# Performance work log

Hardware: AMD Instinct MI355X
Metric: run time of the kernel (lower is better)

Reference implementation:

```python
import jax, jax.numpy as jnp
import numpy as np

B = 32768          # batch
M = 128            # m_spa, embedding dim
N_TAB = 26         # number of sparse tables
N_ROWS = 100000    # rows per table
LN_BOT = [13, 512, 256, 128]
LN_TOP = [479, 1024, 1024, 1]  # 479 = 128 + 27*26/2

# strictly-lower-triangle indices of the (1+N_TAB) x (1+N_TAB) interaction matrix,
# in the same row-major order as the torch list-comprehension.
_LI, _LJ = np.tril_indices(N_TAB + 1, k=-1)


def _mlp_params(key, ln):
    ws, bs = [], []
    for i in range(len(ln) - 1):
        n, m = ln[i], ln[i + 1]
        key, k1, k2 = jax.random.split(key, 3)
        ws.append(jax.random.normal(k1, (m, n), jnp.float32) * np.sqrt(2.0 / (m + n)))
        bs.append(jax.random.normal(k2, (m,), jnp.float32) * np.sqrt(1.0 / m))
    return ws, bs


def setup_inputs() -> dict:
    key = jax.random.key(0)
    kd, ki, ke, kb, kt = jax.random.split(key, 5)
    dense_x = jax.random.normal(kd, (B, LN_BOT[0]), jnp.float32)
    lS_i = jax.random.randint(ki, (N_TAB, B), 0, N_ROWS, dtype=jnp.int64)
    lS_o = jnp.tile(jnp.arange(B, dtype=jnp.int64), (N_TAB, 1))  # one index per bag
    bound = np.sqrt(1.0 / N_ROWS)
    emb_W = jax.random.uniform(ke, (N_TAB, N_ROWS, M), jnp.float32, -bound, bound)
    bw, bb = _mlp_params(kb, LN_BOT)
    tw, tb = _mlp_params(kt, LN_TOP)
    return {
        "dense_x": dense_x, "lS_i": lS_i, "lS_o": lS_o, "emb_W": emb_W,
        "bot_w0": bw[0], "bot_b0": bb[0], "bot_w1": bw[1], "bot_b1": bb[1],
        "bot_w2": bw[2], "bot_b2": bb[2],
        "top_w0": tw[0], "top_b0": tb[0], "top_w1": tw[1], "top_b1": tb[1],
        "top_w2": tw[2], "top_b2": tb[2],
    }


def _forward(dense_x, lS_i, emb_W,
             bot_w0, bot_b0, bot_w1, bot_b1, bot_w2, bot_b2,
             top_w0, top_b0, top_w1, top_b1, top_w2, top_b2):
    # bottom MLP (all ReLU, sigmoid_bot = -1)
    x = jax.nn.relu(dense_x @ bot_w0.T + bot_b0)
    x = jax.nn.relu(x @ bot_w1.T + bot_b1)
    x = jax.nn.relu(x @ bot_w2.T + bot_b2)                      # [B, M]
    # embedding lookups; offsets are arange(B) -> sum-pool of a single index == gather
    ly = jax.vmap(lambda W, idx: W[idx])(emb_W, lS_i)           # [N_TAB, B, M]
    # pairwise feature interaction
    T = jnp.concatenate([x[:, None, :], jnp.transpose(ly, (1, 0, 2))], axis=1)  # [B, 27, M]
    Z = jnp.einsum('bid,bjd->bij', T, T)                        # [B, 27, 27]
    Zflat = Z[:, _LI, _LJ]                                      # [B, 351]
    R = jnp.concatenate([x, Zflat], axis=1)                     # [B, 479]
    # top MLP (ReLU, ReLU, Sigmoid at layer index 2)
    z = jax.nn.relu(R @ top_w0.T + top_b0)
    z = jax.nn.relu(z @ top_w1.T + top_b1)
    p = jax.nn.sigmoid(z @ top_w2.T + top_b2)                   # [B, 1]
    return p  # loss_threshold == 0.0 -> no clamp


def reference(dense_x, lS_i, lS_o, emb_W,
              bot_w0, bot_b0, bot_w1, bot_b1, bot_w2, bot_b2,
              top_w0, top_b0, top_w1, top_b1, top_w2, top_b2):
    del lS_o  # offsets = arange(B): one index per bag, pooling is identity
    return _forward(dense_x, lS_i, emb_W,
                    bot_w0, bot_b0, bot_w1, bot_b1, bot_w2, bot_b2,
                    top_w0, top_b0, top_w1, top_b1, top_w2, top_b2)
```

## Files before the change

### kernel.cpp

```cpp
#include <hip/hip_runtime.h>

typedef unsigned short u16;
typedef unsigned int   u32;
typedef __attribute__((ext_vector_type(4))) float f32x4;
typedef __attribute__((ext_vector_type(8))) short bf16x8;
typedef __attribute__((ext_vector_type(4))) unsigned short u16x4;

__device__ __forceinline__ u16 f2bf(float f) {
  u32 u = __float_as_uint(f);
  u = (u + 0x7FFFu + ((u >> 16) & 1u)) >> 16;
  return (u16)u;
}
__device__ __forceinline__ float bf2f(u16 h) {
  return __uint_as_float(((u32)h) << 16);
}

#define GLDS16(gptr, lptr)                                      \
  __builtin_amdgcn_global_load_lds(                             \
      (const __attribute__((address_space(1))) void*)(gptr),    \
      (__attribute__((address_space(3))) void*)(lptr), 16, 0, 0)

#define BARRIER                                                 \
  do {                                                          \
    asm volatile("" ::: "memory");                              \
    __builtin_amdgcn_s_barrier();                               \
    asm volatile("" ::: "memory");                              \
  } while (0)
#define WAITLGKM0 asm volatile("s_waitcnt lgkmcnt(0)" ::: "memory")
#define WAITVM2   asm volatile("s_waitcnt vmcnt(2)" ::: "memory")
#define WAITVM0   asm volatile("s_waitcnt vmcnt(0)" ::: "memory")
#define PRIO1 __builtin_amdgcn_s_setprio(1)
#define PRIO0 __builtin_amdgcn_s_setprio(0)

#define PREP_TOTAL (6656 + 131072 + 32768 + 524288 + 1048576 + 32768)
__global__ __launch_bounds__(256) void prep(
    const float* __restrict__ bw0, const float* __restrict__ bw1,
    const float* __restrict__ bw2, const float* __restrict__ tw0,
    const float* __restrict__ tw1,
    float* __restrict__ w0T, u16* __restrict__ W1B, u16* __restrict__ W2B,
    u16* __restrict__ TW0B, u16* __restrict__ TW1B, float* __restrict__ DOT) {
  int i = blockIdx.x * 256 + threadIdx.x;
  if (i < 6656) {
    int k = i >> 9, n = i & 511;
    w0T[i] = bw0[n * 13 + k];
    return;
  }
  i -= 6656;
  if (i < 131072) { W1B[i] = f2bf(bw1[i]); return; }
  i -= 131072;
  if (i < 32768) { W2B[i] = f2bf(bw2[i]); return; }
  i -= 32768;
  if (i < 524288) {
    int r = i >> 9, k = i & 511;
    TW0B[i] = (k < 479) ? f2bf(tw0[r * 479 + k]) : (u16)0;
    return;
  }
  i -= 524288;
  if (i < 1048576) { TW1B[i] = f2bf(tw1[i]); return; }
  i -= 1048576;
  if (i < 32768) DOT[i] = 0.f;
}

__global__ __launch_bounds__(256) void bot0(const float* __restrict__ dense,
                                            const float* __restrict__ w0T,
                                            const float* __restrict__ b0,
                                            u16* __restrict__ x1) {
  const int t = blockIdx.x * 256 + threadIdx.x;
  const int b = t >> 9, n = t & 511;
  const float* dr = dense + (size_t)b * 13;
  float s = b0[n];
#pragma unroll
  for (int k = 0; k < 13; ++k) s = fmaf(dr[k], w0T[k * 512 + n], s);
  x1[t] = f2bf(fmaxf(s, 0.f));
}

__global__ __launch_bounds__(256) void gemm_bt_relu(
    const u16* __restrict__ A, const u16* __restrict__ W,
    const float* __restrict__ bias, u16* __restrict__ C,
    int M, int N, int K) {
  __shared__ u16 Al[128 * 32];
  __shared__ u16 Bl[128 * 32];
  const int tid = threadIdx.x;
  const int wave = tid >> 6, lane = tid & 63;
  const int ntn = N >> 7;
  const int bm = blockIdx.x / ntn, bn = blockIdx.x % ntn;
  const int wm = (wave >> 1) << 6, wn = (wave & 1) << 6;
  const int fr = lane & 15, fq = lane >> 4;

  const int srow = wave * 16 + (lane >> 2);
  const int scol = (lane & 3) * 8;
  const u16* ag0 = A + (size_t)(bm * 128 + srow) * K + scol;
  const u16* ag1 = ag0 + (size_t)64 * K;
  const u16* wg0 = W + (size_t)(bn * 128 + srow) * K + scol;
  const u16* wg1 = wg0 + (size_t)64 * K;
  u16* la0 = &Al[(wave * 16) * 32];
  u16* la1 = &Al[(64 + wave * 16) * 32];
  u16* lb0 = &Bl[(wave * 16) * 32];
  u16* lb1 = &Bl[(64 + wave * 16) * 32];

  f32x4 acc[4][4] = {};

  for (int kt = 0; kt < K; kt += 32) {
    __syncthreads();
    GLDS16(ag0 + kt, la0);
    GLDS16(ag1 + kt, la1);
    GLDS16(wg0 + kt, lb0);
    GLDS16(wg1 + kt, lb1);
    __syncthreads();
    bf16x8 af[4], bfv[4];
#pragma unroll
    for (int i = 0; i < 4; ++i) {
      af[i]  = *(const bf16x8*)&Al[(wm + i * 16 + fr) * 32 + fq * 8];
      bfv[i] = *(const bf16x8*)&Bl[(wn + i * 16 + fr) * 32 + fq * 8];
    }
#pragma unroll
    for (int i = 0; i < 4; ++i)
#pragma unroll
      for (int j = 0; j < 4; ++j)
        acc[i][j] = __builtin_amdgcn_mfma_f32_16x16x32_bf16(af[i], bfv[j],
                                                            acc[i][j], 0, 0, 0);
  }

  const int crow0 = bm * 128 + wm, ccol0 = bn * 128 + wn;
#pragma unroll
  for (int i = 0; i < 4; ++i) {
#pragma unroll
    for (int j = 0; j < 4; ++j) {
      const int col = ccol0 + j * 16 + fr;
      const float bv = bias[col];
#pragma unroll
      for (int rr = 0; rr < 4; ++rr) {
        const int row = crow0 + i * 16 + fq * 4 + rr;
        float v = acc[i][j][rr] + bv;
        v = fmaxf(v, 0.f);
        C[(size_t)row * N + col] = f2bf(v);
      }
    }
  }
}

#define LDA4(dst, FB, BUFE)                                                    \
  _Pragma("unroll") for (int f = 0; f < 4; ++f)                                \
  _Pragma("unroll") for (int ks = 0; ks < 2; ++ks)                             \
    dst[f][ks] = *(const bf16x8*)&lds[(BUFE) +                                 \
        (wm * 128 + (FB) * 16 + f * 16 + fr) * 64 +                            \
        ((ks * 4 + fq) ^ fr7) * 8];

#define LDB2(dst, GB, BUFE)                                                    \
  _Pragma("unroll") for (int g = 0; g < 2; ++g)                                \
  _Pragma("unroll") for (int ks = 0; ks < 2; ++ks)                             \
    dst[g][ks] = *(const bf16x8*)&lds[(BUFE) + 16384 +                         \
        (wn * 64 + (GB) * 16 + g * 16 + fr) * 64 +                             \
        ((ks * 4 + fq) ^ fr7) * 8];

#define MFQ(FB, GB, va, vb)                                                    \
  _Pragma("unroll") for (int f = 0; f < 4; ++f)                                \
  _Pragma("unroll") for (int g = 0; g < 2; ++g)                                \
  _Pragma("unroll") for (int ks = 0; ks < 2; ++ks)                             \
    acc[(FB) + f][(GB) + g] = __builtin_amdgcn_mfma_f32_16x16x32_bf16(         \
        va[f][ks], vb[g][ks], acc[(FB) + f][(GB) + g], 0, 0, 0);

template <int FUSE>
__global__ __launch_bounds__(512, 2) void gemm256(
    const u16* __restrict__ Ap, const u16* __restrict__ Wp,
    const float* __restrict__ bias, u16* __restrict__ C,
    const float* __restrict__ w2, float* __restrict__ dotacc,
    int N, int K) {
  __shared__ u16 lds[65536];
  const int tid = threadIdx.x;
  const int wave = tid >> 6, lane = tid & 63;
  const int wm = wave >> 2, wn = wave & 3;
  const int fr = lane & 15, fq = lane >> 4, fr7 = fr & 7;
  const int nkt = K >> 6, NP = nkt >> 1;

  const int nwg = gridDim.x;
  const int swz = (blockIdx.x & 7) * (nwg >> 3) + (blockIdx.x >> 3);
  const int ntn = N >> 8;
  const int bm = swz / ntn, bn = swz % ntn;

  auto stageH = [&](int tile, int half) {
    const int isB = half >> 1;
    const int h128 = half & 1;
    const u16* mat = isB ? Wp : Ap;
    const int brow0 = (isB ? bn : bm) * 256 + h128 * 128;
    u16* lb = lds + (tile & 1) * 32768 + isB * 16384 + h128 * 8192 + wave * 512;
    const int sl = lane >> 3;
    const int ch = (lane & 7) ^ sl;
    const u16* g = mat + (size_t)(brow0 + wave * 8 + sl) * K + tile * 64 + ch * 8;
    GLDS16(g, lb);
    GLDS16(g + (size_t)64 * K, lb + 4096);
  };

  f32x4 acc[8][4] = {};

  stageH(0, 0); stageH(0, 1); stageH(0, 2); stageH(0, 3);
  stageH(1, 0);
  WAITVM2;
  BARRIER;

  for (int p = 0; p < NP; ++p) {
    const int todd = 2 * p + 1, t2 = 2 * p + 2, t3 = 2 * p + 3;
    const bool last = (p == NP - 1);
    bf16x8 va[4][2], vb0[2][2], vb1[2][2];

    LDA4(va, 0, 0); LDB2(vb0, 0, 0);
    stageH(todd, 1);
    BARRIER; WAITLGKM0; PRIO1; MFQ(0, 0, va, vb0); PRIO0; BARRIER;
    LDB2(vb1, 2, 0);
    stageH(todd, 2);
    BARRIER; WAITLGKM0; PRIO1; MFQ(0, 2, va, vb1); PRIO0; BARRIER;
    LDA4(va, 4, 0);
    stageH(todd, 3);
    BARRIER; WAITLGKM0; PRIO1; MFQ(4, 0, va, vb0); PRIO0; BARRIER;
    if (t2 < nkt) stageH(t2, 0);
    BARRIER; PRIO1; MFQ(4, 2, va, vb1); PRIO0;
    if (last) { WAITVM0; } else { WAITVM2; }
    BARRIER;

    LDA4(va, 0, 32768); LDB2(vb0, 0, 32768);
    if (t2 < nkt) stageH(t2, 1);
    BARRIER; WAITLGKM0; PRIO1; MFQ(0, 0, va, vb0); PRIO0; BARRIER;
    LDB2(vb1, 2, 32768);
    if (t2 < nkt) stageH(t2, 2);
    BARRIER; WAITLGKM0; PRIO1; MFQ(0, 2, va, vb1); PRIO0; BARRIER;
    LDA4(va, 4, 32768);
    if (t2 < nkt) stageH(t2, 3);
    BARRIER; WAITLGKM0; PRIO1; MFQ(4, 0, va, vb0); PRIO0; BARRIER;
    if (t3 < nkt) stageH(t3, 0);
    BARRIER; PRIO1; MFQ(4, 2, va, vb1); PRIO0;
    if (!last) { WAITVM2; }
    BARRIER;
  }

  const int r0 = bm * 256 + wm * 128;
  const int c0 = bn * 256 + wn * 64;
  if (FUSE) {
    float bv[4], wv[4];
#pragma unroll
    for (int g = 0; g < 4; ++g) {
      const int col = c0 + g * 16 + fr;
      bv[g] = bias[col];
      wv[g] = w2[col];
    }
#pragma unroll
    for (int f = 0; f < 8; ++f) {
#pragma unroll
      for (int rr = 0; rr < 4; ++rr) {
        float s = 0.f;
#pragma unroll
        for (int g = 0; g < 4; ++g)
          s += fmaxf(acc[f][g][rr] + bv[g], 0.f) * wv[g];
#pragma unroll
        for (int off = 8; off >= 1; off >>= 1) s += __shfl_xor(s, off, 64);
        if (fr == 0)
          atomicAdd(&dotacc[r0 + f * 16 + fq * 4 + rr], s);
      }
    }
  } else {
#pragma unroll
    for (int g = 0; g < 4; ++g) {
      const int col = c0 + g * 16 + fr;
      const float bvv = bias[col];
#pragma unroll
      for (int f = 0; f < 8; ++f)
#pragma unroll
        for (int rr = 0; rr < 4; ++rr) {
          const int row = r0 + f * 16 + fq * 4 + rr;
          C[(size_t)row * N + col] = f2bf(fmaxf(acc[f][g][rr] + bvv, 0.f));
        }
    }
  }
}

__global__ __launch_bounds__(256) void interact(const float* __restrict__ emb,
                                                const int* __restrict__ lsi,
                                                const u16* __restrict__ x3,
                                                u16* __restrict__ R) {
  __shared__ u16 lds[4 * 32 * 128];
  const int tid = threadIdx.x;
  const int b0 = blockIdx.x * 4;

  {
    u32* lz = (u32*)lds;
#pragma unroll
    for (int z = 0; z < 5; ++z) {
      int i = z * 256 + tid;
      int s = i / 320, o = i - s * 320;
      lz[s * 2048 + 1728 + o] = 0u;
    }
  }
  if (tid < 64) {
    int s = tid >> 4, l = tid & 15;
    *(bf16x8*)&lds[(s * 32) * 128 + l * 8] =
        *(const bf16x8*)&x3[(size_t)(b0 + s) * 128 + l * 8];
  }
  {
    const int lane32 = tid & 31;
    const int item0 = tid >> 5;
#pragma unroll
    for (int p = 0; p < 13; ++p) {
      int w = p * 8 + item0;
      int s = w / 26, t = w - s * 26;
      int idx = lsi[t * 32768 + b0 + s];
      const float* er = emb + ((size_t)t * 100000 + (size_t)idx) * 128 + lane32 * 4;
      f32x4 u = *(const f32x4*)er;
      u16x4 q;
      q[0] = f2bf(u[0]); q[1] = f2bf(u[1]); q[2] = f2bf(u[2]); q[3] = f2bf(u[3]);
      int r = t + 1;
      int chunk = (lane32 >> 1) ^ (r & 7);
      *(u16x4*)&lds[(s * 32 + r) * 128 + chunk * 8 + (lane32 & 1) * 4] = q;
    }
  }
  __syncthreads();

  const int wave = tid >> 6, lane = tid & 63;
  const int fr = lane & 15, fq = lane >> 4;
  const u16* ls = &lds[wave * 4096];
  u16* Rb = R + (size_t)(b0 + wave) * 512;

  *(u32*)&Rb[lane * 2] = *(const u32*)&ls[lane * 2];
  if (lane < 33) Rb[479 + lane] = 0;

  bf16x8 tf[2][4];
#pragma unroll
  for (int mi = 0; mi < 2; ++mi) {
    const int r = mi * 16 + fr;
#pragma unroll
    for (int ks = 0; ks < 4; ++ks) {
      const int chunk = (ks * 4 + fq) ^ (r & 7);
      tf[mi][ks] = *(const bf16x8*)&ls[r * 128 + chunk * 8];
    }
  }

  f32x4 acc[2][2] = {};
#pragma unroll
  for (int ks = 0; ks < 4; ++ks)
#pragma unroll
    for (int mi = 0; mi < 2; ++mi)
#pragma unroll
      for (int ni = 0; ni < 2; ++ni)
        acc[mi][ni] = __builtin_amdgcn_mfma_f32_16x16x32_bf16(
            tf[mi][ks], tf[ni][ks], acc[mi][ni], 0, 0, 0);

#pragma unroll
  for (int mi = 0; mi < 2; ++mi)
#pragma unroll
    for (int ni = 0; ni < 2; ++ni)
#pragma unroll
      for (int rr = 0; rr < 4; ++rr) {
        const int i = mi * 16 + fq * 4 + rr;
        const int j = ni * 16 + fr;
        if (i < 27 && j < i)
          Rb[128 + (i * (i - 1)) / 2 + j] = f2bf(acc[mi][ni][rr]);
      }
}

__global__ __launch_bounds__(256) void sig_k(const float* __restrict__ accv,
                                             const float* __restrict__ b2,
                                             float* __restrict__ out, int n) {
  int i = blockIdx.x * 256 + threadIdx.x;
  if (i < n) out[i] = 1.f / (1.f + expf(-(accv[i] + b2[0])));
}

extern "C" void kernel_launch(void* const* d_in, const int* in_sizes, int n_in,
                              void* d_out, int out_size, void* d_ws,
                              size_t ws_size, hipStream_t stream) {
  const float* dense = (const float*)d_in[0];
  const int*   lsi   = (const int*)d_in[1];
  const float* emb = (const float*)d_in[3];
  const float* bw0 = (const float*)d_in[4];
  const float* bb0 = (const float*)d_in[5];
  const float* bw1 = (const float*)d_in[6];
  const float* bb1 = (const float*)d_in[7];
  const float* bw2 = (const float*)d_in[8];
  const float* bb2 = (const float*)d_in[9];
  const float* tw0 = (const float*)d_in[10];
  const float* tb0 = (const float*)d_in[11];
  const float* tw1 = (const float*)d_in[12];
  const float* tb1 = (const float*)d_in[13];
  const float* tw2 = (const float*)d_in[14];
  const float* tb2 = (const float*)d_in[15];

  char* ws = (char*)d_ws;
  u16* W1B  = (u16*)ws; ws += (size_t)256 * 512 * 2;
  u16* W2B  = (u16*)ws; ws += (size_t)128 * 256 * 2;
  u16* TW0B = (u16*)ws; ws += (size_t)1024 * 512 * 2;
  u16* TW1B = (u16*)ws; ws += (size_t)1024 * 1024 * 2;
  float* DOT = (float*)ws; ws += (size_t)32768 * 4;
  float* W0T = (float*)ws; ws += (size_t)13 * 512 * 4;
  u16* X3   = (u16*)ws; ws += (size_t)32768 * 128 * 2;
  u16* SA   = (u16*)ws; ws += (size_t)32768 * 1024 * 2;
  u16* SB   = (u16*)ws; ws += (size_t)32768 * 1024 * 2;

  prep<<<(PREP_TOTAL + 255) / 256, 256, 0, stream>>>(
      bw0, bw1, bw2, tw0, tw1, W0T, W1B, W2B, TW0B, TW1B, DOT);

  bot0<<<65536, 256, 0, stream>>>(dense, W0T, bb0, SA);
  gemm_bt_relu<<<512, 256, 0, stream>>>(SA, W1B, bb1, SB, 32768, 256, 512);
  gemm_bt_relu<<<256, 256, 0, stream>>>(SB, W2B, bb2, X3, 32768, 128, 256);
  interact<<<8192, 256, 0, stream>>>(emb, lsi, X3, SA);
  gemm256<0><<<512, 512, 0, stream>>>(SA, TW0B, tb0, SB, nullptr, nullptr,
                                      1024, 512);
  gemm256<1><<<512, 512, 0, stream>>>(SB, TW1B, tb1, nullptr, tw2, DOT,
                                      1024, 1024);
  sig_k<<<128, 256, 0, stream>>>(DOT, tb2, (float*)d_out, 32768);
}
```

Before: 310.6 us.

## Pipeline interaction and top-MLP GEMMs across batch chunks in combined launches

Splits the batch into four chunks of 8192 rows. Each combined 'pipe' kernel runs the interaction for the next chunk, the first top-MLP GEMM for the current chunk and the fused second GEMM plus dot product for the previous chunk, picking the role by block index. This overlaps the memory-bound embedding gather with the compute-bound GEMMs and fills the GPU better between stages. In exchange the top GEMMs use the smaller 128-tile body instead of the 256-tile kernel in the pipelined stages, and there are more launches.

```diff
diff --git a/kernel.cpp b/kernel.cpp
--- a/kernel.cpp
+++ b/kernel.cpp
@@ -74,16 +74,16 @@
   x1[t] = f2bf(fmaxf(s, 0.f));
 }
 
-__global__ __launch_bounds__(256) void gemm_bt_relu(
-    const u16* __restrict__ A, const u16* __restrict__ W,
+template <int FUSE>
+__device__ __forceinline__ void g128_body(
+    u16* lds, const u16* __restrict__ A, const u16* __restrict__ W,
     const float* __restrict__ bias, u16* __restrict__ C,
-    int M, int N, int K) {
-  __shared__ u16 Al[128 * 32];
-  __shared__ u16 Bl[128 * 32];
+    const float* __restrict__ w2, float* __restrict__ dotacc,
+    int bm, int bn, int N, int K) {
+  u16* Al = lds;
+  u16* Bl = lds + 4096;
   const int tid = threadIdx.x;
   const int wave = tid >> 6, lane = tid & 63;
-  const int ntn = N >> 7;
-  const int bm = blockIdx.x / ntn, bn = blockIdx.x % ntn;
   const int wm = (wave >> 1) << 6, wn = (wave & 1) << 6;
   const int fr = lane & 15, fq = lane >> 4;
 
@@ -122,21 +122,172 @@
   }
 
   const int crow0 = bm * 128 + wm, ccol0 = bn * 128 + wn;
-#pragma unroll
-  for (int i = 0; i < 4; ++i) {
+  if (FUSE) {
+    float bv[4], wv[4];
 #pragma unroll
     for (int j = 0; j < 4; ++j) {
       const int col = ccol0 + j * 16 + fr;
-      const float bv = bias[col];
+      bv[j] = bias[col];
+      wv[j] = w2[col];
+    }
+#pragma unroll
+    for (int i = 0; i < 4; ++i)
 #pragma unroll
       for (int rr = 0; rr < 4; ++rr) {
-        const int row = crow0 + i * 16 + fq * 4 + rr;
-        float v = acc[i][j][rr] + bv;
-        v = fmaxf(v, 0.f);
-        C[(size_t)row * N + col] = f2bf(v);
+        float s = 0.f;
+#pragma unroll
+        for (int j = 0; j < 4; ++j)
+          s += fmaxf(acc[i][j][rr] + bv[j], 0.f) * wv[j];
+#pragma unroll
+        for (int off = 8; off >= 1; off >>= 1) s += __shfl_xor(s, off, 64);
+        if (fr == 0)
+          atomicAdd(&dotacc[crow0 + i * 16 + fq * 4 + rr], s);
       }
-    }
-  }
+  } else {
+#pragma unroll
+    for (int i = 0; i < 4; ++i)
+#pragma unroll
+      for (int j = 0; j < 4; ++j) {
+        const int col = ccol0 + j * 16 + fr;
+        const float bvv = bias[col];
+#pragma unroll
+        for (int rr = 0; rr < 4; ++rr) {
+          const int row = crow0 + i * 16 + fq * 4 + rr;
+          C[(size_t)row * N + col] = f2bf(fmaxf(acc[i][j][rr] + bvv, 0.f));
+        }
+      }
+  }
+}
+
+__global__ __launch_bounds__(256) void gemm_bt_relu(
+    const u16* __restrict__ A, const u16* __restrict__ W,
+    const float* __restrict__ bias, u16* __restrict__ C, int N, int K) {
+  __shared__ u16 lds[8192];
+  const int ntn = N >> 7;
+  g128_body<0>(lds, A, W, bias, C, nullptr, nullptr, blockIdx.x / ntn,
+               blockIdx.x % ntn, N, K);
+}
+
+__device__ __forceinline__ void interact_body(u16* lds,
+                                              const float* __restrict__ emb,
+                                              const int* __restrict__ lsi,
+                                              const u16* __restrict__ x3,
+                                              u16* __restrict__ R, int b0) {
+  const int tid = threadIdx.x;
+  {
+    u32* lz = (u32*)lds;
+#pragma unroll
+    for (int z = 0; z < 5; ++z) {
+      int i = z * 256 + tid;
+      int s = i / 320, o = i - s * 320;
+      lz[s * 2048 + 1728 + o] = 0u;
+    }
+  }
+  if (tid < 64) {
+    int s = tid >> 4, l = tid & 15;
+    *(bf16x8*)&lds[(s * 32) * 128 + l * 8] =
+        *(const bf16x8*)&x3[(size_t)(b0 + s) * 128 + l * 8];
+  }
+  {
+    const int lane32 = tid & 31;
+    const int item0 = tid >> 5;
+#pragma unroll
+    for (int p = 0; p < 13; ++p) {
+      int w = p * 8 + item0;
+      int s = w / 26, t = w - s * 26;
+      int idx = lsi[t * 32768 + b0 + s];
+      const float* er =
+          emb + ((size_t)t * 100000 + (size_t)idx) * 128 + lane32 * 4;
+      f32x4 u = *(const f32x4*)er;
+      u16x4 q;
+      q[0] = f2bf(u[0]); q[1] = f2bf(u[1]); q[2] = f2bf(u[2]); q[3] = f2bf(u[3]);
+      int r = t + 1;
+      int chunk = (lane32 >> 1) ^ (r & 7);
+      *(u16x4*)&lds[(s * 32 + r) * 128 + chunk * 8 + (lane32 & 1) * 4] = q;
+    }
+  }
+  __syncthreads();
+
+  const int wave = tid >> 6, lane = tid & 63;
+  const int fr = lane & 15, fq = lane >> 4;
+  const u16* ls = &lds[wave * 4096];
+  u16* Rb = R + (size_t)(b0 + wave) * 512;
+
+  *(u32*)&Rb[lane * 2] = *(const u32*)&ls[lane * 2];
+  if (lane < 33) Rb[479 + lane] = 0;
+
+  bf16x8 tf[2][4];
+#pragma unroll
+  for (int mi = 0; mi < 2; ++mi) {
+    const int r = mi * 16 + fr;
+#pragma unroll
+    for (int ks = 0; ks < 4; ++ks) {
+      const int chunk = (ks * 4 + fq) ^ (r & 7);
+      tf[mi][ks] = *(const bf16x8*)&ls[r * 128 + chunk * 8];
+    }
+  }
+
+  f32x4 acc[2][2] = {};
+#pragma unroll
+  for (int ks = 0; ks < 4; ++ks)
+#pragma unroll
+    for (int mi = 0; mi < 2; ++mi)
+#pragma unroll
+      for (int ni = 0; ni < 2; ++ni)
+        acc[mi][ni] = __builtin_amdgcn_mfma_f32_16x16x32_bf16(
+            tf[mi][ks], tf[ni][ks], acc[mi][ni], 0, 0, 0);
+
+#pragma unroll
+  for (int mi = 0; mi < 2; ++mi)
+#pragma unroll
+    for (int ni = 0; ni < 2; ++ni)
+#pragma unroll
+      for (int rr = 0; rr < 4; ++rr) {
+        const int i = mi * 16 + fq * 4 + rr;
+        const int j = ni * 16 + fr;
+        if (i < 27 && j < i)
+          Rb[128 + (i * (i - 1)) / 2 + j] = f2bf(acc[mi][ni][rr]);
+      }
+}
+
+__global__ __launch_bounds__(256) void interact_k(const float* __restrict__ emb,
+                                                  const int* __restrict__ lsi,
+                                                  const u16* __restrict__ x3,
+                                                  u16* __restrict__ R,
+                                                  int bOff) {
+  __shared__ u16 lds[16384];
+  interact_body(lds, emb, lsi, x3, R, bOff + blockIdx.x * 4);
+}
+
+__global__ __launch_bounds__(256) void pipe(
+    const float* __restrict__ emb, const int* __restrict__ lsi,
+    const u16* __restrict__ x3, u16* __restrict__ R, int ibase,
+    int iA, int nZ1, int nZ2,
+    const u16* __restrict__ A1, u16* __restrict__ C1,
+    const u16* __restrict__ W1, const float* __restrict__ b1,
+    const u16* __restrict__ A2, const u16* __restrict__ W2,
+    const float* __restrict__ b2, const float* __restrict__ w2v,
+    float* __restrict__ dot) {
+  __shared__ u16 lds[16384];
+  int bid = blockIdx.x;
+  if (bid < iA) {
+    interact_body(lds, emb, lsi, x3, R, ibase + bid * 4);
+    return;
+  }
+  bid -= iA;
+  if (bid < nZ1) {
+    g128_body<0>(lds, A1, W1, b1, C1, nullptr, nullptr, bid >> 3, bid & 7,
+                 1024, 512);
+    return;
+  }
+  bid -= nZ1;
+  if (bid < nZ2) {
+    g128_body<1>(lds, A2, W2, b2, nullptr, w2v, dot, bid >> 3, bid & 7,
+                 1024, 1024);
+    return;
+  }
+  bid -= nZ2;
+  interact_body(lds, emb, lsi, x3, R, ibase + (iA + bid) * 4);
 }
 
 #define LDA4(dst, FB, BUFE)                                                    \
@@ -270,89 +421,6 @@
         }
     }
   }
-}
-
-__global__ __launch_bounds__(256) void interact(const float* __restrict__ emb,
-                                                const int* __restrict__ lsi,
-                                                const u16* __restrict__ x3,
-                                                u16* __restrict__ R) {
-  __shared__ u16 lds[4 * 32 * 128];
-  const int tid = threadIdx.x;
-  const int b0 = blockIdx.x * 4;
-
-  {
-    u32* lz = (u32*)lds;
-#pragma unroll
-    for (int z = 0; z < 5; ++z) {
-      int i = z * 256 + tid;
-      int s = i / 320, o = i - s * 320;
-      lz[s * 2048 + 1728 + o] = 0u;
-    }
-  }
-  if (tid < 64) {
-    int s = tid >> 4, l = tid & 15;
-    *(bf16x8*)&lds[(s * 32) * 128 + l * 8] =
-        *(const bf16x8*)&x3[(size_t)(b0 + s) * 128 + l * 8];
-  }
-  {
-    const int lane32 = tid & 31;
-    const int item0 = tid >> 5;
-#pragma unroll
-    for (int p = 0; p < 13; ++p) {
-      int w = p * 8 + item0;
-      int s = w / 26, t = w - s * 26;
-      int idx = lsi[t * 32768 + b0 + s];
-      const float* er = emb + ((size_t)t * 100000 + (size_t)idx) * 128 + lane32 * 4;
-      f32x4 u = *(const f32x4*)er;
-      u16x4 q;
-      q[0] = f2bf(u[0]); q[1] = f2bf(u[1]); q[2] = f2bf(u[2]); q[3] = f2bf(u[3]);
-      int r = t + 1;
-      int chunk = (lane32 >> 1) ^ (r & 7);
-      *(u16x4*)&lds[(s * 32 + r) * 128 + chunk * 8 + (lane32 & 1) * 4] = q;
-    }
-  }
-  __syncthreads();
-
-  const int wave = tid >> 6, lane = tid & 63;
-  const int fr = lane & 15, fq = lane >> 4;
-  const u16* ls = &lds[wave * 4096];
-  u16* Rb = R + (size_t)(b0 + wave) * 512;
-
-  *(u32*)&Rb[lane * 2] = *(const u32*)&ls[lane * 2];
-  if (lane < 33) Rb[479 + lane] = 0;
-
-  bf16x8 tf[2][4];
-#pragma unroll
-  for (int mi = 0; mi < 2; ++mi) {
-    const int r = mi * 16 + fr;
-#pragma unroll
-    for (int ks = 0; ks < 4; ++ks) {
-      const int chunk = (ks * 4 + fq) ^ (r & 7);
-      tf[mi][ks] = *(const bf16x8*)&ls[r * 128 + chunk * 8];
-    }
-  }
-
-  f32x4 acc[2][2] = {};
-#pragma unroll
-  for (int ks = 0; ks < 4; ++ks)
-#pragma unroll
-    for (int mi = 0; mi < 2; ++mi)
-#pragma unroll
-      for (int ni = 0; ni < 2; ++ni)
-        acc[mi][ni] = __builtin_amdgcn_mfma_f32_16x16x32_bf16(
-            tf[mi][ks], tf[ni][ks], acc[mi][ni], 0, 0, 0);
-
-#pragma unroll
-  for (int mi = 0; mi < 2; ++mi)
-#pragma unroll
-    for (int ni = 0; ni < 2; ++ni)
-#pragma unroll
-      for (int rr = 0; rr < 4; ++rr) {
-        const int i = mi * 16 + fq * 4 + rr;
-        const int j = ni * 16 + fr;
-        if (i < 27 && j < i)
-          Rb[128 + (i * (i - 1)) / 2 + j] = f2bf(acc[mi][ni][rr]);
-      }
 }
 
 __global__ __launch_bounds__(256) void sig_k(const float* __restrict__ accv,
@@ -392,16 +460,32 @@
   u16* SA   = (u16*)ws; ws += (size_t)32768 * 1024 * 2;
   u16* SB   = (u16*)ws; ws += (size_t)32768 * 1024 * 2;
 
+  const int CH = 8192;
+  auto SAc = [&](int c) { return SA + (size_t)c * CH * 512; };
+  auto SBc = [&](int c) { return SB + (size_t)c * CH * 1024; };
+
   prep<<<(PREP_TOTAL + 255) / 256, 256, 0, stream>>>(
       bw0, bw1, bw2, tw0, tw1, W0T, W1B, W2B, TW0B, TW1B, DOT);
 
   bot0<<<65536, 256, 0, stream>>>(dense, W0T, bb0, SA);
-  gemm_bt_relu<<<512, 256, 0, stream>>>(SA, W1B, bb1, SB, 32768, 256, 512);
-  gemm_bt_relu<<<256, 256, 0, stream>>>(SB, W2B, bb2, X3, 32768, 128, 256);
-  interact<<<8192, 256, 0, stream>>>(emb, lsi, X3, SA);
-  gemm256<0><<<512, 512, 0, stream>>>(SA, TW0B, tb0, SB, nullptr, nullptr,
-                                      1024, 512);
-  gemm256<1><<<512, 512, 0, stream>>>(SB, TW1B, tb1, nullptr, tw2, DOT,
-                                      1024, 1024);
+  gemm_bt_relu<<<512, 256, 0, stream>>>(SA, W1B, bb1, SB, 256, 512);
+  gemm_bt_relu<<<256, 256, 0, stream>>>(SB, W2B, bb2, X3, 128, 256);
+
+  interact_k<<<2048, 256, 0, stream>>>(emb, lsi, X3, SA, 0);
+  pipe<<<512 + 512 + 0 + 1536, 256, 0, stream>>>(
+      emb, lsi, X3, SA, 1 * CH, 512, 512, 0,
+      SAc(0), SBc(0), TW0B, tb0, nullptr, TW1B, tb1, tw2, nullptr);
+  pipe<<<512 + 512 + 512 + 1536, 256, 0, stream>>>(
+      emb, lsi, X3, SA, 2 * CH, 512, 512, 512,
+      SAc(1), SBc(1), TW0B, tb0, SBc(0), TW1B, tb1, tw2, DOT + 0 * CH);
+  pipe<<<512 + 512 + 512 + 1536, 256, 0, stream>>>(
+      emb, lsi, X3, SA, 3 * CH, 512, 512, 512,
+      SAc(2), SBc(2), TW0B, tb0, SBc(1), TW1B, tb1, tw2, DOT + 1 * CH);
+  gemm256<0><<<128, 512, 0, stream>>>(SAc(3), TW0B, tb0, SBc(3), nullptr,
+                                      nullptr, 1024, 512);
+  gemm256<1><<<128, 512, 0, stream>>>(SBc(2), TW1B, tb1, nullptr, tw2,
+                                      DOT + 2 * CH, 1024, 1024);
+  gemm256<1><<<128, 512, 0, stream>>>(SBc(3), TW1B, tb1, nullptr, tw2,
+                                      DOT + 3 * CH, 1024, 1024);
   sig_k<<<128, 256, 0, stream>>>(DOT, tb2, (float*)d_out, 32768);
 }
```

After: 361.3 us. 1.16x slower.

## Fuse last bottom-MLP layer into interaction kernel using scalar FMA

Applied to the files above, without the earlier changes.

Removes the separate 256->128 bottom GEMM launch and its X3 intermediate by computing that layer inside the interaction kernel. Each thread computes two output columns for one sample with scalar bf16->fp32 FMAs, reading the activation row and two weight rows from global memory. This saves one launch and a round trip through global memory, but replaces an MFMA GEMM with scalar math and re-reads the 64KB weight matrix in every block. It also adds a long serial dot-product loop before the barrier.

```diff
diff --git a/kernel.cpp b/kernel.cpp
--- a/kernel.cpp
+++ b/kernel.cpp
@@ -272,10 +272,12 @@
   }
 }
 
-__global__ __launch_bounds__(256) void interact(const float* __restrict__ emb,
-                                                const int* __restrict__ lsi,
-                                                const u16* __restrict__ x3,
-                                                u16* __restrict__ R) {
+__global__ __launch_bounds__(256) void interact3(const float* __restrict__ emb,
+                                                 const int* __restrict__ lsi,
+                                                 const u16* __restrict__ x2,
+                                                 const u16* __restrict__ W2B,
+                                                 const float* __restrict__ b2v,
+                                                 u16* __restrict__ R) {
   __shared__ u16 lds[4 * 32 * 128];
   const int tid = threadIdx.x;
   const int b0 = blockIdx.x * 4;
@@ -289,11 +291,6 @@
       lz[s * 2048 + 1728 + o] = 0u;
     }
   }
-  if (tid < 64) {
-    int s = tid >> 4, l = tid & 15;
-    *(bf16x8*)&lds[(s * 32) * 128 + l * 8] =
-        *(const bf16x8*)&x3[(size_t)(b0 + s) * 128 + l * 8];
-  }
   {
     const int lane32 = tid & 31;
     const int item0 = tid >> 5;
@@ -302,7 +299,8 @@
       int w = p * 8 + item0;
       int s = w / 26, t = w - s * 26;
       int idx = lsi[t * 32768 + b0 + s];
-      const float* er = emb + ((size_t)t * 100000 + (size_t)idx) * 128 + lane32 * 4;
+      const float* er =
+          emb + ((size_t)t * 100000 + (size_t)idx) * 128 + lane32 * 4;
       f32x4 u = *(const f32x4*)er;
       u16x4 q;
       q[0] = f2bf(u[0]); q[1] = f2bf(u[1]); q[2] = f2bf(u[2]); q[3] = f2bf(u[3]);
@@ -311,6 +309,32 @@
       *(u16x4*)&lds[(s * 32 + r) * 128 + chunk * 8 + (lane32 & 1) * 4] = q;
     }
   }
+  {
+    const int s = tid >> 6, c0 = (tid & 63) * 2;
+    const u16* xr = x2 + (size_t)(b0 + s) * 256;
+    const u16* wr0 = W2B + (size_t)c0 * 256;
+    const u16* wr1 = wr0 + 256;
+    float a0 = b2v[c0], a1 = b2v[c0 + 1];
+#pragma unroll
+    for (int k = 0; k < 256; k += 8) {
+      bf16x8 xv  = *(const bf16x8*)&xr[k];
+      bf16x8 wv0 = *(const bf16x8*)&wr0[k];
+      bf16x8 wv1 = *(const bf16x8*)&wr1[k];
+#pragma unroll
+      for (int j = 0; j < 8; ++j) {
+        const float xf = bf2f((u16)xv[j]);
+        a0 = fmaf(xf, bf2f((u16)wv0[j]), a0);
+        a1 = fmaf(xf, bf2f((u16)wv1[j]), a1);
+      }
+    }
+    const u16 q0 = f2bf(fmaxf(a0, 0.f));
+    const u16 q1 = f2bf(fmaxf(a1, 0.f));
+    lds[(s * 32) * 128 + c0] = q0;
+    lds[(s * 32) * 128 + c0 + 1] = q1;
+    u16* Rb = R + (size_t)(b0 + s) * 512;
+    Rb[c0] = q0;
+    Rb[c0 + 1] = q1;
+  }
   __syncthreads();
 
   const int wave = tid >> 6, lane = tid & 63;
@@ -318,7 +342,6 @@
   const u16* ls = &lds[wave * 4096];
   u16* Rb = R + (size_t)(b0 + wave) * 512;
 
-  *(u32*)&Rb[lane * 2] = *(const u32*)&ls[lane * 2];
   if (lane < 33) Rb[479 + lane] = 0;
 
   bf16x8 tf[2][4];
@@ -388,7 +411,6 @@
   u16* TW1B = (u16*)ws; ws += (size_t)1024 * 1024 * 2;
   float* DOT = (float*)ws; ws += (size_t)32768 * 4;
   float* W0T = (float*)ws; ws += (size_t)13 * 512 * 4;
-  u16* X3   = (u16*)ws; ws += (size_t)32768 * 128 * 2;
   u16* SA   = (u16*)ws; ws += (size_t)32768 * 1024 * 2;
   u16* SB   = (u16*)ws; ws += (size_t)32768 * 1024 * 2;
 
@@ -397,8 +419,7 @@
 
   bot0<<<65536, 256, 0, stream>>>(dense, W0T, bb0, SA);
   gemm_bt_relu<<<512, 256, 0, stream>>>(SA, W1B, bb1, SB, 32768, 256, 512);
-  gemm_bt_relu<<<256, 256, 0, stream>>>(SB, W2B, bb2, X3, 32768, 128, 256);
-  interact<<<8192, 256, 0, stream>>>(emb, lsi, X3, SA);
+  interact3<<<8192, 256, 0, stream>>>(emb, lsi, SB, W2B, bb2, SA);
   gemm256<0><<<512, 512, 0, stream>>>(SA, TW0B, tb0, SB, nullptr, nullptr,
                                       1024, 512);
   gemm256<1><<<512, 512, 0, stream>>>(SB, TW1B, tb1, nullptr, tw2, DOT,
```

New measurement: 654.0 us. 111% more time.
